# Optimization experiments

Measured on AMD Instinct MI355X. Metric: run time of the kernel, lower is better.

## Reference

```python
import jax, jax.numpy as jnp
import numpy as np

# Config matching init_kwargs / input_specs
B, H, S, D = 4, 16, 4096, 64
BLK = 16          # sparsity_block
W = 32            # num_local_blocks (banded causal layout: block i attends blocks i-W+1..i)


def setup_inputs() -> dict:
    key = jax.random.key(0)
    kq, kk, kv = jax.random.split(key, 3)
    query = jax.random.normal(kq, (B, H, S, D), dtype=jnp.float16)
    k = jax.random.normal(kk, (B, H, S, D), dtype=jnp.float16)
    value = jax.random.normal(kv, (B, H, S, D), dtype=jnp.float16)
    return {"query": query, "key": k, "value": value}


def reference(query, key, value):
    b, h, s, d = query.shape
    nb = s // BLK
    scale = 1.0 / np.sqrt(d)

    qb = query.reshape(b, h, nb, BLK, d)
    kb = key.reshape(b, h, nb, BLK, d)
    vb = value.reshape(b, h, nb, BLK, d)

    # Banded causal block layout: for query block i, kv block indices i-W+1 .. i
    i = jnp.arange(nb)[:, None]                    # [nb,1]
    w = jnp.arange(W)[None, :]                     # [1,W]
    kv_idx = i - (W - 1) + w                       # [nb,W]
    valid = kv_idx >= 0
    idxc = jnp.clip(kv_idx, 0, nb - 1)

    kg = kb[:, :, idxc]                            # [B,H,nb,W,BLK,D] gathered K blocks
    vg = vb[:, :, idxc]                            # [B,H,nb,W,BLK,D]

    # SDD: block-sparse QK^T, only active blocks are computed
    scores = jnp.einsum('bhnqd,bhnwkd->bhnqwk', qb, kg).astype(jnp.float32) * scale

    # causal + validity mask on global token positions
    q_pos = (jnp.arange(nb) * BLK)[:, None, None, None] + jnp.arange(BLK)[None, :, None, None]  # [nb,BLK,1,1]
    k_pos = (kv_idx * BLK)[:, None, :, None] + jnp.arange(BLK)[None, None, None, :]             # [nb,1,W,BLK]
    mask = (k_pos <= q_pos) & valid[:, None, :, None]
    scores = jnp.where(mask, scores, -jnp.inf)

    # sparse softmax over all active key positions of each query row
    p = jax.nn.softmax(scores.reshape(b, h, nb, BLK, W * BLK), axis=-1)
    p = p.reshape(b, h, nb, BLK, W, BLK).astype(jnp.float16)

    # DSD: sparse-probabilities x dense-V
    out = jnp.einsum('bhnqwk,bhnwkd->bhnqd', p, vg)
    return out.reshape(b, h, s, d)
```

## Files before the change

### kernel.cpp

```cpp
#include <hip/hip_runtime.h>

#define SS 4096
#define DD 64
#define WW 32
#define NEG (-1e30f)
#define LOG2E 1.44269504f

typedef _Float16 half8_t __attribute__((ext_vector_type(8)));
typedef float float4_t __attribute__((ext_vector_type(4)));

#define VSTR 40
#define KSTR 68

static __device__ __forceinline__ unsigned pack2(float a, float b) {
  union { _Float16 h[2]; unsigned u; } x;
  x.h[0] = (_Float16)a;
  x.h[1] = (_Float16)b;
  return x.u;
}

static __device__ __forceinline__ half8_t cvt8(const float* p) {
  float4_t a = *(const float4_t*)p;
  float4_t b = *(const float4_t*)(p + 4);
  half8_t h;
#pragma unroll
  for (int r = 0; r < 4; ++r) {
    h[r] = (_Float16)a[r];
    h[r + 4] = (_Float16)b[r];
  }
  return h;
}

static __device__ __forceinline__ half8_t lds_frag(const unsigned short* p) {
  union { half8_t h; uint2 u[2]; } x;
  x.u[0] = *(const uint2*)p;
  x.u[1] = *(const uint2*)(p + 4);
  return x.h;
}

__global__ __launch_bounds__(256, 4)
void sparse_attn_kernel(const float* __restrict__ Q,
                        const float* __restrict__ K,
                        const float* __restrict__ V,
                        float* __restrict__ O) {
  __shared__ __align__(16) unsigned short kl[2][64 * KSTR];
  __shared__ __align__(16) unsigned short vl[2][2][64 * VSTR];

  const int lin = blockIdx.x;
  const int xcd = lin & 7;
  const int logical = (lin >> 3) + xcd * ((int)gridDim.x >> 3);
  const int bh = logical >> 6;
  const int i0 = (logical & 63) * 4;

  const int tid = threadIdx.x;
  const int wave = tid >> 6;
  const int lane = tid & 63;
  const int t = lane & 15;
  const int q = lane >> 4;

  const size_t base = (size_t)bh * SS * DD;
  const float* Qb = Q + base;
  const float* Kb = K + base;
  const float* Vb = V + base;

  const int i = i0 + wave;

  const float* qrow = Qb + (size_t)(i * 16 + t) * DD;
  half8_t qf0 = cvt8(qrow + q * 8);
  half8_t qf1 = cvt8(qrow + 32 + q * 8);

  const int prow0 = ((t >> 2) << 3) + (t & 3);

  float4_t accO[4];
#pragma unroll
  for (int c = 0; c < 4; ++c) accO[c] = {0.f, 0.f, 0.f, 0.f};
  float m_run = NEG;
  float l_run = 0.0f;

  const int lo_blk = (i0 - (WW - 1)) > 0 ? (i0 - (WW - 1)) : 0;
  const int Ulo = lo_blk >> 2;
  const int Uhi = (i0 + 3) >> 2;
  const int nit = Uhi - Ulo + 1;

  const int kr_ = tid >> 2;
  const int kc_ = (tid & 3) * 16;
  const int n0s = (tid >> 5) * 4;
  const int sds = (tid & 31) * 2;

  float4_t kv[4];
  float2 vv[8];

  auto load_raw = [&](int U) {
    const float* ks = Kb + (size_t)(U * 64 + kr_) * DD + kc_;
#pragma unroll
    for (int ii = 0; ii < 4; ++ii) kv[ii] = *(const float4_t*)(ks + ii * 4);
#pragma unroll
    for (int p = 0; p < 2; ++p)
#pragma unroll
      for (int rr = 0; rr < 4; ++rr)
        vv[p * 4 + rr] =
            *(const float2*)(Vb + (size_t)(U * 64 + p * 32 + n0s + rr) * DD + sds);
  };

  auto store_stage = [&](int bf) {
    unsigned short* kd = &kl[bf][kr_ * KSTR + kc_];
#pragma unroll
    for (int ii = 0; ii < 4; ++ii) {
      uint2 w;
      w.x = pack2(kv[ii][0], kv[ii][1]);
      w.y = pack2(kv[ii][2], kv[ii][3]);
      *(uint2*)(kd + ii * 4) = w;
    }
#pragma unroll
    for (int p = 0; p < 2; ++p) {
      uint2 wlo, whi;
      wlo.x = pack2(vv[p * 4 + 0].x, vv[p * 4 + 1].x);
      wlo.y = pack2(vv[p * 4 + 2].x, vv[p * 4 + 3].x);
      whi.x = pack2(vv[p * 4 + 0].y, vv[p * 4 + 1].y);
      whi.y = pack2(vv[p * 4 + 2].y, vv[p * 4 + 3].y);
      *(uint2*)&vl[bf][p][sds * VSTR + n0s] = wlo;
      *(uint2*)&vl[bf][p][(sds + 1) * VSTR + n0s] = whi;
    }
  };

  load_raw(Ulo);

  for (int it = 0; it < nit; ++it) {
    const int U = Ulo + it;
    const int bf = it & 1;
    store_stage(bf);
    __syncthreads();
    if (it + 1 < nit) load_raw(U + 1);

    if (4 * U >= i - 34) {
      float4_t st[4];
#pragma unroll
      for (int g = 0; g < 4; ++g) st[g] = {0.f, 0.f, 0.f, 0.f};
#pragma unroll
      for (int p = 0; p < 2; ++p) {
#pragma unroll
        for (int ro = 0; ro < 2; ++ro) {
          const int rowb = p * 32 + prow0 + ro * 4;
          const unsigned short* kp = &kl[bf][rowb * KSTR + q * 8];
          half8_t kf0 = lds_frag(kp);
          half8_t kf1 = lds_frag(kp + 32);
          st[p * 2 + ro] =
              __builtin_amdgcn_mfma_f32_16x16x32_f16(kf0, qf0, st[p * 2 + ro], 0, 0, 0);
          st[p * 2 + ro] =
              __builtin_amdgcn_mfma_f32_16x16x32_f16(kf1, qf1, st[p * 2 + ro], 0, 0, 0);
        }
      }

      float s[4][4];
#pragma unroll
      for (int p = 0; p < 2; ++p) {
        const int jj = 4 * U + 2 * p + (q >> 1);
        const bool bad = (jj < i - (WW - 1)) || (jj > i);
        const bool dg = (jj == i);
        const int kr = (q & 1) << 3;
#pragma unroll
        for (int ro = 0; ro < 2; ++ro)
#pragma unroll
          for (int r = 0; r < 4; ++r) {
            float v = st[p * 2 + ro][r] * 0.125f;
            if (bad || (dg && (kr + ro * 4 + r > t))) v = NEG;
            s[p * 2 + ro][r] = v;
          }
      }
      float vmax = NEG;
#pragma unroll
      for (int g = 0; g < 4; ++g)
#pragma unroll
        for (int r = 0; r < 4; ++r) vmax = fmaxf(vmax, s[g][r]);
      vmax = fmaxf(vmax, __shfl_xor(vmax, 16));
      vmax = fmaxf(vmax, __shfl_xor(vmax, 32));
      const float m_new = fmaxf(m_run, vmax);
      const float alpha = __builtin_exp2f((m_run - m_new) * LOG2E);

      float rs = 0.f;
#pragma unroll
      for (int g = 0; g < 4; ++g)
#pragma unroll
        for (int r = 0; r < 4; ++r) {
          s[g][r] = __builtin_exp2f((s[g][r] - m_new) * LOG2E);
          rs += s[g][r];
        }
      rs += __shfl_xor(rs, 16);
      rs += __shfl_xor(rs, 32);
      l_run = l_run * alpha + rs;
      m_run = m_new;

      half8_t pb0, pb1;
#pragma unroll
      for (int r = 0; r < 4; ++r) {
        pb0[r] = (_Float16)s[0][r];
        pb0[r + 4] = (_Float16)s[1][r];
        pb1[r] = (_Float16)s[2][r];
        pb1[r + 4] = (_Float16)s[3][r];
      }

      const unsigned short* v0 = vl[bf][0];
      const unsigned short* v1 = vl[bf][1];
#pragma unroll
      for (int c = 0; c < 4; ++c) {
#pragma unroll
        for (int r = 0; r < 4; ++r) accO[c][r] *= alpha;
        half8_t va0 = lds_frag(&v0[(c * 16 + t) * VSTR + q * 8]);
        half8_t va1 = lds_frag(&v1[(c * 16 + t) * VSTR + q * 8]);
        accO[c] = __builtin_amdgcn_mfma_f32_16x16x32_f16(va0, pb0, accO[c], 0, 0, 0);
        accO[c] = __builtin_amdgcn_mfma_f32_16x16x32_f16(va1, pb1, accO[c], 0, 0, 0);
      }
    }
  }

  const float inv_l = 1.0f / l_run;
  float* orow = O + base + (size_t)(i * 16 + t) * DD;
#pragma unroll
  for (int c = 0; c < 4; ++c) {
    float4_t ov;
#pragma unroll
    for (int r = 0; r < 4; ++r) ov[r] = accO[c][r] * inv_l;
    *(float4_t*)(orow + c * 16 + q * 4) = ov;
  }
}

extern "C" void kernel_launch(void* const* d_in, const int* in_sizes, int n_in,
                              void* d_out, int out_size, void* d_ws, size_t ws_size,
                              hipStream_t stream) {
  const float* Q = (const float*)d_in[0];
  const float* K = (const float*)d_in[1];
  const float* V = (const float*)d_in[2];
  float* O = (float*)d_out;
  sparse_attn_kernel<<<dim3(4096), dim3(256), 0, stream>>>(Q, K, V, O);
}
```

Measured before the change: 271.4 us.

## Widen workgroups to 8 query blocks, swizzle LDS, defer softmax rescaling

Each workgroup now processes 8 query blocks with 512 threads, so every staged 64-row K/V tile is shared by more waves and the redundant K/V loads per query block drop. The padded LDS layouts are replaced by XOR-swizzled ones, which allows 16-byte fragment reads without bank conflicts. The log2e factor is folded into the score scale, masking is skipped for interior tiles, and the running-max rescale is done only when the max grows past a threshold, which removes most alpha multiplies. Conversions now use packed cvt_pkrtz. In exchange, occupancy and register pressure change and the probabilities are exposed to a larger dynamic range before the deferred rescale.

```diff
diff --git a/kernel.cpp b/kernel.cpp
--- a/kernel.cpp
+++ b/kernel.cpp
@@ -4,53 +4,52 @@
 #define DD 64
 #define WW 32
 #define NEG (-1e30f)
-#define LOG2E 1.44269504f
+#define CSCALE 0.1803368801f
+#define DEFER_THR 8.0f
 
 typedef _Float16 half8_t __attribute__((ext_vector_type(8)));
+typedef __fp16 fp16x2_t __attribute__((ext_vector_type(2)));
 typedef float float4_t __attribute__((ext_vector_type(4)));
 
-#define VSTR 40
-#define KSTR 68
-
-static __device__ __forceinline__ unsigned pack2(float a, float b) {
-  union { _Float16 h[2]; unsigned u; } x;
-  x.h[0] = (_Float16)a;
-  x.h[1] = (_Float16)b;
-  return x.u;
+static __device__ __forceinline__ unsigned pk(float a, float b) {
+  fp16x2_t h = __builtin_amdgcn_cvt_pkrtz(a, b);
+  return __builtin_bit_cast(unsigned, h);
 }
 
 static __device__ __forceinline__ half8_t cvt8(const float* p) {
   float4_t a = *(const float4_t*)p;
   float4_t b = *(const float4_t*)(p + 4);
-  half8_t h;
-#pragma unroll
-  for (int r = 0; r < 4; ++r) {
-    h[r] = (_Float16)a[r];
-    h[r + 4] = (_Float16)b[r];
-  }
-  return h;
-}
-
-static __device__ __forceinline__ half8_t lds_frag(const unsigned short* p) {
-  union { half8_t h; uint2 u[2]; } x;
-  x.u[0] = *(const uint2*)p;
-  x.u[1] = *(const uint2*)(p + 4);
+  union { half8_t h; unsigned u[4]; } x;
+  x.u[0] = pk(a[0], a[1]);
+  x.u[1] = pk(a[2], a[3]);
+  x.u[2] = pk(b[0], b[1]);
+  x.u[3] = pk(b[2], b[3]);
   return x.h;
 }
 
-__global__ __launch_bounds__(256, 4)
+static __device__ __forceinline__ half8_t lds_frag16(const unsigned short* p) {
+  union { half8_t h; uint4 u; } x;
+  x.u = *(const uint4*)p;
+  return x.h;
+}
+
+static __device__ __forceinline__ int ksig(int r) {
+  return ((r & 3) ^ ((r >> 3) & 3)) | ((r & 2) << 1);
+}
+
+__global__ __launch_bounds__(512, 6)
 void sparse_attn_kernel(const float* __restrict__ Q,
                         const float* __restrict__ K,
                         const float* __restrict__ V,
                         float* __restrict__ O) {
-  __shared__ __align__(16) unsigned short kl[2][64 * KSTR];
-  __shared__ __align__(16) unsigned short vl[2][2][64 * VSTR];
+  __shared__ __align__(16) unsigned short kl[2][64 * 64];
+  __shared__ __align__(16) unsigned short vl[2][2][64 * 32];
 
   const int lin = blockIdx.x;
   const int xcd = lin & 7;
   const int logical = (lin >> 3) + xcd * ((int)gridDim.x >> 3);
-  const int bh = logical >> 6;
-  const int i0 = (logical & 63) * 4;
+  const int bh = logical >> 5;
+  const int i0 = (logical & 31) * 8;
 
   const int tid = threadIdx.x;
   const int wave = tid >> 6;
@@ -66,10 +65,19 @@
   const int i = i0 + wave;
 
   const float* qrow = Qb + (size_t)(i * 16 + t) * DD;
-  half8_t qf0 = cvt8(qrow + q * 8);
-  half8_t qf1 = cvt8(qrow + 32 + q * 8);
+  const half8_t qf0 = cvt8(qrow + q * 8);
+  const half8_t qf1 = cvt8(qrow + 32 + q * 8);
 
   const int prow0 = ((t >> 2) << 3) + (t & 3);
+  int koff[2][2];
+#pragma unroll
+  for (int p = 0; p < 2; ++p)
+#pragma unroll
+    for (int ro = 0; ro < 2; ++ro) {
+      const int rowb = p * 32 + prow0 + ro * 4;
+      koff[p][ro] = rowb * 64 + ((q ^ ksig(rowb)) << 3);
+    }
+  const int vslot8 = (q ^ ((t >> 1) & 3)) << 3;
 
   float4_t accO[4];
 #pragma unroll
@@ -79,94 +87,99 @@
 
   const int lo_blk = (i0 - (WW - 1)) > 0 ? (i0 - (WW - 1)) : 0;
   const int Ulo = lo_blk >> 2;
-  const int Uhi = (i0 + 3) >> 2;
+  const int Uhi = (i0 + 7) >> 2;
   const int nit = Uhi - Ulo + 1;
 
-  const int kr_ = tid >> 2;
-  const int kc_ = (tid & 3) * 16;
-  const int n0s = (tid >> 5) * 4;
-  const int sds = (tid & 31) * 2;
-
-  float4_t kv[4];
-  float2 vv[8];
-
-  auto load_raw = [&](int U) {
-    const float* ks = Kb + (size_t)(U * 64 + kr_) * DD + kc_;
-#pragma unroll
-    for (int ii = 0; ii < 4; ++ii) kv[ii] = *(const float4_t*)(ks + ii * 4);
-#pragma unroll
-    for (int p = 0; p < 2; ++p)
-#pragma unroll
-      for (int rr = 0; rr < 4; ++rr)
-        vv[p * 4 + rr] =
-            *(const float2*)(Vb + (size_t)(U * 64 + p * 32 + n0s + rr) * DD + sds);
+  const int kr_ = tid >> 3;
+  const int kc8 = tid & 7;
+  const int kstoff = kr_ * 64 + ((kc8 ^ ksig(kr_)) << 3);
+
+  const int vpair = tid >> 8;
+  const int vdl = tid & 31;
+  const int vn0 = ((tid >> 5) & 7) * 4;
+  const int vstoff = (vdl * 2) * 32 + (vn0 ^ ((vdl & 3) << 3));
+
+  const float* kg = Kb + (size_t)(Ulo * 64 + kr_) * DD + kc8 * 8;
+  const float* vg = Vb + (size_t)(Ulo * 64 + vpair * 32 + vn0) * DD + vdl * 2;
+
+  float4_t kv[2];
+  float2 vv[4];
+
+  auto load_raw = [&]() {
+    kv[0] = *(const float4_t*)kg;
+    kv[1] = *(const float4_t*)(kg + 4);
+#pragma unroll
+    for (int rr = 0; rr < 4; ++rr) vv[rr] = *(const float2*)(vg + rr * DD);
+    kg += 64 * DD;
+    vg += 64 * DD;
   };
 
   auto store_stage = [&](int bf) {
-    unsigned short* kd = &kl[bf][kr_ * KSTR + kc_];
-#pragma unroll
-    for (int ii = 0; ii < 4; ++ii) {
-      uint2 w;
-      w.x = pack2(kv[ii][0], kv[ii][1]);
-      w.y = pack2(kv[ii][2], kv[ii][3]);
-      *(uint2*)(kd + ii * 4) = w;
-    }
-#pragma unroll
-    for (int p = 0; p < 2; ++p) {
-      uint2 wlo, whi;
-      wlo.x = pack2(vv[p * 4 + 0].x, vv[p * 4 + 1].x);
-      wlo.y = pack2(vv[p * 4 + 2].x, vv[p * 4 + 3].x);
-      whi.x = pack2(vv[p * 4 + 0].y, vv[p * 4 + 1].y);
-      whi.y = pack2(vv[p * 4 + 2].y, vv[p * 4 + 3].y);
-      *(uint2*)&vl[bf][p][sds * VSTR + n0s] = wlo;
-      *(uint2*)&vl[bf][p][(sds + 1) * VSTR + n0s] = whi;
-    }
+    uint4 w;
+    w.x = pk(kv[0][0], kv[0][1]);
+    w.y = pk(kv[0][2], kv[0][3]);
+    w.z = pk(kv[1][0], kv[1][1]);
+    w.w = pk(kv[1][2], kv[1][3]);
+    *(uint4*)&kl[bf][kstoff] = w;
+    uint2 wlo, whi;
+    wlo.x = pk(vv[0].x, vv[1].x);
+    wlo.y = pk(vv[2].x, vv[3].x);
+    whi.x = pk(vv[0].y, vv[1].y);
+    whi.y = pk(vv[2].y, vv[3].y);
+    unsigned short* vd = &vl[bf][vpair][vstoff];
+    *(uint2*)vd = wlo;
+    *(uint2*)(vd + 32) = whi;
   };
 
-  load_raw(Ulo);
+  load_raw();
 
   for (int it = 0; it < nit; ++it) {
     const int U = Ulo + it;
     const int bf = it & 1;
     store_stage(bf);
     __syncthreads();
-    if (it + 1 < nit) load_raw(U + 1);
-
-    if (4 * U >= i - 34) {
+    if (it + 1 < nit) load_raw();
+
+    if (4 * U <= i && 4 * U >= i - 34) {
       float4_t st[4];
 #pragma unroll
       for (int g = 0; g < 4; ++g) st[g] = {0.f, 0.f, 0.f, 0.f};
 #pragma unroll
-      for (int p = 0; p < 2; ++p) {
+      for (int p = 0; p < 2; ++p)
 #pragma unroll
         for (int ro = 0; ro < 2; ++ro) {
-          const int rowb = p * 32 + prow0 + ro * 4;
-          const unsigned short* kp = &kl[bf][rowb * KSTR + q * 8];
-          half8_t kf0 = lds_frag(kp);
-          half8_t kf1 = lds_frag(kp + 32);
+          half8_t kf0 = lds_frag16(&kl[bf][koff[p][ro]]);
+          half8_t kf1 = lds_frag16(&kl[bf][koff[p][ro] ^ 32]);
           st[p * 2 + ro] =
               __builtin_amdgcn_mfma_f32_16x16x32_f16(kf0, qf0, st[p * 2 + ro], 0, 0, 0);
           st[p * 2 + ro] =
               __builtin_amdgcn_mfma_f32_16x16x32_f16(kf1, qf1, st[p * 2 + ro], 0, 0, 0);
         }
+
+      float s[4][4];
+      if ((4 * U < i - (WW - 1)) || (4 * U + 3 >= i)) {
+#pragma unroll
+        for (int p = 0; p < 2; ++p) {
+          const int jj = 4 * U + 2 * p + (q >> 1);
+          const bool bad = (jj < i - (WW - 1)) || (jj > i);
+          const bool dg = (jj == i);
+          const int kr = (q & 1) << 3;
+#pragma unroll
+          for (int ro = 0; ro < 2; ++ro)
+#pragma unroll
+            for (int r = 0; r < 4; ++r) {
+              float v = st[p * 2 + ro][r] * CSCALE;
+              if (bad || (dg && (kr + ro * 4 + r > t))) v = NEG;
+              s[p * 2 + ro][r] = v;
+            }
+        }
+      } else {
+#pragma unroll
+        for (int g = 0; g < 4; ++g)
+#pragma unroll
+          for (int r = 0; r < 4; ++r) s[g][r] = st[g][r] * CSCALE;
       }
 
-      float s[4][4];
-#pragma unroll
-      for (int p = 0; p < 2; ++p) {
-        const int jj = 4 * U + 2 * p + (q >> 1);
-        const bool bad = (jj < i - (WW - 1)) || (jj > i);
-        const bool dg = (jj == i);
-        const int kr = (q & 1) << 3;
-#pragma unroll
-        for (int ro = 0; ro < 2; ++ro)
-#pragma unroll
-          for (int r = 0; r < 4; ++r) {
-            float v = st[p * 2 + ro][r] * 0.125f;
-            if (bad || (dg && (kr + ro * 4 + r > t))) v = NEG;
-            s[p * 2 + ro][r] = v;
-          }
-      }
       float vmax = NEG;
 #pragma unroll
       for (int g = 0; g < 4; ++g)
@@ -174,41 +187,49 @@
         for (int r = 0; r < 4; ++r) vmax = fmaxf(vmax, s[g][r]);
       vmax = fmaxf(vmax, __shfl_xor(vmax, 16));
       vmax = fmaxf(vmax, __shfl_xor(vmax, 32));
-      const float m_new = fmaxf(m_run, vmax);
-      const float alpha = __builtin_exp2f((m_run - m_new) * LOG2E);
+
+      if (__any(vmax > m_run + DEFER_THR)) {
+        const float m_new = fmaxf(m_run, vmax);
+        const float alpha = __builtin_exp2f(m_run - m_new);
+        l_run *= alpha;
+#pragma unroll
+        for (int c = 0; c < 4; ++c)
+#pragma unroll
+          for (int r = 0; r < 4; ++r) accO[c][r] *= alpha;
+        m_run = m_new;
+      }
 
       float rs = 0.f;
 #pragma unroll
       for (int g = 0; g < 4; ++g)
 #pragma unroll
         for (int r = 0; r < 4; ++r) {
-          s[g][r] = __builtin_exp2f((s[g][r] - m_new) * LOG2E);
+          s[g][r] = __builtin_exp2f(s[g][r] - m_run);
           rs += s[g][r];
         }
       rs += __shfl_xor(rs, 16);
       rs += __shfl_xor(rs, 32);
-      l_run = l_run * alpha + rs;
-      m_run = m_new;
-
-      half8_t pb0, pb1;
-#pragma unroll
-      for (int r = 0; r < 4; ++r) {
-        pb0[r] = (_Float16)s[0][r];
-        pb0[r + 4] = (_Float16)s[1][r];
-        pb1[r] = (_Float16)s[2][r];
-        pb1[r + 4] = (_Float16)s[3][r];
-      }
+      l_run += rs;
+
+      union { half8_t h; unsigned u[4]; } pb0, pb1;
+      pb0.u[0] = pk(s[0][0], s[0][1]);
+      pb0.u[1] = pk(s[0][2], s[0][3]);
+      pb0.u[2] = pk(s[1][0], s[1][1]);
+      pb0.u[3] = pk(s[1][2], s[1][3]);
+      pb1.u[0] = pk(s[2][0], s[2][1]);
+      pb1.u[1] = pk(s[2][2], s[2][3]);
+      pb1.u[2] = pk(s[3][0], s[3][1]);
+      pb1.u[3] = pk(s[3][2], s[3][3]);
 
       const unsigned short* v0 = vl[bf][0];
       const unsigned short* v1 = vl[bf][1];
 #pragma unroll
       for (int c = 0; c < 4; ++c) {
-#pragma unroll
-        for (int r = 0; r < 4; ++r) accO[c][r] *= alpha;
-        half8_t va0 = lds_frag(&v0[(c * 16 + t) * VSTR + q * 8]);
-        half8_t va1 = lds_frag(&v1[(c * 16 + t) * VSTR + q * 8]);
-        accO[c] = __builtin_amdgcn_mfma_f32_16x16x32_f16(va0, pb0, accO[c], 0, 0, 0);
-        accO[c] = __builtin_amdgcn_mfma_f32_16x16x32_f16(va1, pb1, accO[c], 0, 0, 0);
+        const int voff = (c * 16 + t) * 32 + vslot8;
+        half8_t va0 = lds_frag16(&v0[voff]);
+        half8_t va1 = lds_frag16(&v1[voff]);
+        accO[c] = __builtin_amdgcn_mfma_f32_16x16x32_f16(va0, pb0.h, accO[c], 0, 0, 0);
+        accO[c] = __builtin_amdgcn_mfma_f32_16x16x32_f16(va1, pb1.h, accO[c], 0, 0, 0);
       }
     }
   }
@@ -231,5 +252,5 @@
   const float* K = (const float*)d_in[1];
   const float* V = (const float*)d_in[2];
   float* O = (float*)d_out;
-  sparse_attn_kernel<<<dim3(4096), dim3(256), 0, stream>>>(Q, K, V, O);
-}
+  sparse_attn_kernel<<<dim3(2048), dim3(512), 0, stream>>>(Q, K, V, O);
+}
```

After: 297.6 us. 9.6% more time.
